# Optimization experiments

Hardware: AMD Instinct MI355X
Metric: run time of the kernel (lower is better)

The kernel has to match this reference:

```python
import jax, jax.numpy as jnp
import numpy as np

N, T = 32, 1024
CIN, H, O, F2 = 64, 128, 16, 16  # F2 = 2 * FiLMed_layers
EPS = 1e-5
SLOPE = 0.01  # nn.LeakyReLU default


def _leaky(x):
    return jnp.where(x >= 0, x, SLOPE * x)


def _ln(x, gamma, beta):
    # x: (N,T,O,H); gamma,beta: (O,H) -> broadcast per channel
    mu = jnp.mean(x, axis=-1, keepdims=True)
    var = jnp.mean(jnp.square(x - mu), axis=-1, keepdims=True)
    return (x - mu) * jax.lax.rsqrt(var + EPS) * gamma + beta


def setup_inputs() -> dict:
    key = jax.random.key(0)
    ks = jax.random.split(key, 7)
    s0 = 1.0 / np.sqrt(CIN)
    s1 = 1.0 / np.sqrt(H)
    return {
        "x": jax.random.normal(ks[0], (N, T, CIN), jnp.float32),
        "W0": jax.random.uniform(ks[1], (O, H, CIN), jnp.float32, -s0, s0),
        "b0": jax.random.uniform(ks[2], (O, H), jnp.float32, -s0, s0),
        "g0": jnp.ones((O, H), jnp.float32),
        "be0": jnp.zeros((O, H), jnp.float32),
        "W1": jax.random.uniform(ks[3], (O, H, H), jnp.float32, -s1, s1),
        "b1": jax.random.uniform(ks[4], (O, H), jnp.float32, -s1, s1),
        "g1": jnp.ones((O, H), jnp.float32),
        "be1": jnp.zeros((O, H), jnp.float32),
        "W2": jax.random.uniform(ks[5], (O, F2, H), jnp.float32, -s1, s1),
        "b2": jax.random.uniform(ks[6], (O, F2), jnp.float32, -s1, s1),
    }


def reference(x, W0, b0, g0, be0, W1, b1, g1, be1, W2, b2):
    # Per-channel MLP, vectorized over the O channel axis.
    h = jnp.einsum("ntc,ohc->ntoh", x, W0) + b0          # (N,T,O,H)
    h = _ln(_leaky(h), g0, be0)
    h = jnp.einsum("ntoh,ogh->ntog", h, W1) + b1         # (N,T,O,H)
    h = _ln(_leaky(h), g1, be1)
    out = jnp.einsum("ntoh,ofh->ntof", h, W2) + b2       # (N,T,O,F2)
    out = _leaky(out)
    # torch: stack(dim=1) -> (N,O,T,F2); moveaxis(1,-1) -> (N,T,F2,O)
    return jnp.moveaxis(out, 2, 3)
```

## Files before the change

kernel.cpp:

```cpp
#include <hip/hip_runtime.h>

#define NTOK  32768
#define CIN   64
#define HDIM  128
#define O_CH  16
#define F2    16
#define SLOPE 0.01f
#define EPS   1e-5f

#define SW0_STRIDE 72
#define SW1_STRIDE 136
#define SW2_STRIDE 136
#define SH_STRIDE  136
#define SW0_OFF 0
#define SW1_OFF 9216
#define SW2_OFF (9216 + 17408)
#define WIMG_SHORTS 28800
#define SH_OFF  28800
#define SMEM_TOT (28800 + 64 * SH_STRIDE)

#define WIMG_OFF   0
#define WIMG_BYTES ((size_t)O_CH * WIMG_SHORTS * 2)
#define XBF_OFF    WIMG_BYTES
#define XBF_BYTES  ((size_t)NTOK * CIN * 2)
#define B0F_OFF    (XBF_OFF + XBF_BYTES)
#define B0F_BYTES  ((size_t)O_CH * HDIM * 4)
#define B1F_OFF    (B0F_OFF + B0F_BYTES)
#define B1F_BYTES  ((size_t)O_CH * HDIM * 4)
#define B2F_OFF    (B1F_OFF + B1F_BYTES)
#define B2F_BYTES  ((size_t)O_CH * F2 * 4)

typedef __attribute__((ext_vector_type(8))) short bf16x8;
typedef __attribute__((ext_vector_type(4))) short bf16x4;
typedef __attribute__((ext_vector_type(4))) float f32x4;

__device__ __forceinline__ float b2f(unsigned short u) {
  union { unsigned int i; float f; } v;
  v.i = ((unsigned int)u) << 16;
  return v.f;
}
__device__ __forceinline__ unsigned short f2b(float f) {
  union { float f; unsigned int i; } v;
  v.f = f;
  unsigned int i = v.i;
  unsigned int r = (i + 0x7fffu + ((i >> 16) & 1u)) >> 16;
  return (unsigned short)r;
}
__device__ __forceinline__ float leaky(float t) {
  return (t >= 0.f) ? t : SLOPE * t;
}
__device__ __forceinline__ bf16x8 cvt8(const float* __restrict__ p) {
  float4 a = *(const float4*)p;
  float4 b = *(const float4*)(p + 4);
  bf16x8 r;
  r[0] = (short)f2b(a.x); r[1] = (short)f2b(a.y);
  r[2] = (short)f2b(a.z); r[3] = (short)f2b(a.w);
  r[4] = (short)f2b(b.x); r[5] = (short)f2b(b.y);
  r[6] = (short)f2b(b.z); r[7] = (short)f2b(b.w);
  return r;
}
__device__ __forceinline__ bf16x8 cvt8s(const float* __restrict__ p,
                                        const float* __restrict__ s) {
  bf16x8 r;
#pragma unroll
  for (int i = 0; i < 8; ++i) r[i] = (short)f2b(p[i] * s[i]);
  return r;
}

__device__ __forceinline__ void leaky_ln_store(
    const f32x4* acc, unsigned short* __restrict__ sh,
    int row0, int lo16, int quad) {
  float v[8][4];
  float s1 = 0.f, s2 = 0.f;
#pragma unroll
  for (int nt = 0; nt < 8; ++nt) {
#pragma unroll
    for (int r = 0; r < 4; ++r) {
      float t = leaky(acc[nt][r]);
      v[nt][r] = t;
      s1 += t;
      s2 += t * t;
    }
  }
  s1 += __shfl_xor(s1, 16); s2 += __shfl_xor(s2, 16);
  s1 += __shfl_xor(s1, 32); s2 += __shfl_xor(s2, 32);
  float mu = s1 * (1.0f / 128.0f);
  float var = s2 * (1.0f / 128.0f) - mu * mu;
  float rs = rsqrtf(var + EPS);
#pragma unroll
  for (int nt = 0; nt < 8; ++nt) {
    bf16x4 p;
#pragma unroll
    for (int r = 0; r < 4; ++r)
      p[r] = (short)f2b((v[nt][r] - mu) * rs);
    *(bf16x4*)&sh[(row0 + lo16) * SH_STRIDE + nt * 16 + quad * 4] = p;
  }
}

__global__ __launch_bounds__(256) void prep(
    const float* __restrict__ x,
    const float* __restrict__ W0, const float* __restrict__ b0,
    const float* __restrict__ g0, const float* __restrict__ be0,
    const float* __restrict__ W1, const float* __restrict__ b1,
    const float* __restrict__ g1, const float* __restrict__ be1,
    const float* __restrict__ W2, const float* __restrict__ b2,
    unsigned short* __restrict__ wimg, unsigned short* __restrict__ xbf,
    float* __restrict__ b0f, float* __restrict__ b1f,
    float* __restrict__ b2f) {
  const int bid = blockIdx.x, tid = threadIdx.x;
  if (bid < 16) {
    const int o = bid;
    __shared__ float sg0[HDIM], sbe0[HDIM], sg1[HDIM], sbe1[HDIM];
    if (tid < 128) {
      sg0[tid]  = g0 [o * HDIM + tid];
      sbe0[tid] = be0[o * HDIM + tid];
      sg1[tid]  = g1 [o * HDIM + tid];
      sbe1[tid] = be1[o * HDIM + tid];
    }
    __syncthreads();
    unsigned short* img = wimg + (size_t)o * WIMG_SHORTS;
    const float* w0 = W0 + (size_t)o * HDIM * CIN;
    for (int c = tid; c < (HDIM * CIN) / 8; c += 256) {
      int n = c >> 3, k8 = c & 7;
      *(bf16x8*)&img[SW0_OFF + n * SW0_STRIDE + k8 * 8] = cvt8(w0 + c * 8);
    }
    const float* w1 = W1 + (size_t)o * HDIM * HDIM;
    for (int c = tid; c < (HDIM * HDIM) / 8; c += 256) {
      int n = c >> 4, k8 = c & 15;
      *(bf16x8*)&img[SW1_OFF + n * SW1_STRIDE + k8 * 8] =
          cvt8s(w1 + c * 8, sg0 + k8 * 8);
    }
    const float* w2 = W2 + (size_t)o * F2 * HDIM;
    for (int c = tid; c < (F2 * HDIM) / 8; c += 256) {
      int n = c >> 4, k8 = c & 15;
      *(bf16x8*)&img[SW2_OFF + n * SW2_STRIDE + k8 * 8] =
          cvt8s(w2 + c * 8, sg1 + k8 * 8);
    }
    if (tid < 128) {
      b0f[o * HDIM + tid] = b0[o * HDIM + tid];
      float d = 0.f;
      const float* w1r = w1 + (size_t)tid * HDIM;
      for (int k = 0; k < HDIM; ++k) d += w1r[k] * sbe0[k];
      b1f[o * HDIM + tid] = b1[o * HDIM + tid] + d;
    } else if (tid < 144) {
      int f = tid - 128;
      float d = 0.f;
      const float* w2r = w2 + (size_t)f * HDIM;
      for (int k = 0; k < HDIM; ++k) d += w2r[k] * sbe1[k];
      b2f[o * F2 + f] = b2[o * F2 + f] + d;
    }
  } else {
    int idx = (bid - 16) * 256 + tid;
    *(bf16x8*)&xbf[(size_t)idx * 8] = cvt8(x + (size_t)idx * 8);
  }
}

__global__ __launch_bounds__(256, 2) void film_main(
    const unsigned short* __restrict__ xbf,
    const unsigned short* __restrict__ wimg,
    const float* __restrict__ b0f, const float* __restrict__ b1f,
    const float* __restrict__ b2f,
    float* __restrict__ out) {
  __shared__ unsigned short smem[SMEM_TOT];
  const int tid = threadIdx.x;
  const int c   = blockIdx.x & 7;
  const int o   = (blockIdx.x >> 3) & 15;
  const int q   = blockIdx.x >> 7;
  const int tok0 = (q * 8 + c) * 256;

  {
    const bf16x8* src = (const bf16x8*)(wimg + (size_t)o * WIMG_SHORTS);
    for (int i = tid; i < WIMG_SHORTS / 8; i += 256)
      *(bf16x8*)&smem[i * 8] = src[i];
  }

  const int lane = tid & 63;
  const int wave = tid >> 6;
  const int lo16 = lane & 15;
  const int quad = lane >> 4;
  const int row0 = wave * 16;

  f32x4 bias0[8], bias1[8];
#pragma unroll
  for (int nt = 0; nt < 8; ++nt) {
    bias0[nt] = *(const f32x4*)&b0f[o * HDIM + nt * 16 + quad * 4];
    bias1[nt] = *(const f32x4*)&b1f[o * HDIM + nt * 16 + quad * 4];
  }
  const f32x4 bias2 = *(const f32x4*)&b2f[o * F2 + quad * 4];
  __syncthreads();

  for (int mt = 0; mt < 4; ++mt) {
    const int trow = tok0 + wave * 64 + mt * 16;

    f32x4 acc[8];
#pragma unroll
    for (int nt = 0; nt < 8; ++nt) acc[nt] = bias0[nt];
    {
      const unsigned short* xr = xbf + (size_t)(trow + lo16) * CIN + quad * 8;
#pragma unroll
      for (int ks = 0; ks < 2; ++ks) {
        bf16x8 bx = *(const bf16x8*)(xr + ks * 32);
#pragma unroll
        for (int nt = 0; nt < 8; ++nt) {
          bf16x8 a = *(const bf16x8*)
              &smem[SW0_OFF + (nt * 16 + lo16) * SW0_STRIDE + ks * 32 + quad * 8];
          acc[nt] = __builtin_amdgcn_mfma_f32_16x16x32_bf16(a, bx, acc[nt], 0, 0, 0);
        }
      }
    }
    leaky_ln_store(acc, smem + SH_OFF, row0, lo16, quad);

#pragma unroll
    for (int nt = 0; nt < 8; ++nt) acc[nt] = bias1[nt];
#pragma unroll
    for (int ks = 0; ks < 4; ++ks) {
      bf16x8 bh = *(const bf16x8*)
          &smem[SH_OFF + (row0 + lo16) * SH_STRIDE + ks * 32 + quad * 8];
#pragma unroll
      for (int nt = 0; nt < 8; ++nt) {
        bf16x8 a = *(const bf16x8*)
            &smem[SW1_OFF + (nt * 16 + lo16) * SW1_STRIDE + ks * 32 + quad * 8];
        acc[nt] = __builtin_amdgcn_mfma_f32_16x16x32_bf16(a, bh, acc[nt], 0, 0, 0);
      }
    }
    leaky_ln_store(acc, smem + SH_OFF, row0, lo16, quad);

    f32x4 acc2 = bias2;
#pragma unroll
    for (int ks = 0; ks < 4; ++ks) {
      bf16x8 bh = *(const bf16x8*)
          &smem[SH_OFF + (row0 + lo16) * SH_STRIDE + ks * 32 + quad * 8];
      bf16x8 a = *(const bf16x8*)
          &smem[SW2_OFF + lo16 * SW2_STRIDE + ks * 32 + quad * 8];
      acc2 = __builtin_amdgcn_mfma_f32_16x16x32_bf16(a, bh, acc2, 0, 0, 0);
    }
    {
      const size_t tb = (size_t)(trow + lo16) * (F2 * O_CH);
#pragma unroll
      for (int r = 0; r < 4; ++r)
        out[tb + (quad * 4 + r) * O_CH + o] = leaky(acc2[r]);
    }
  }
}

extern "C" void kernel_launch(void* const* d_in, const int* in_sizes, int n_in,
                              void* d_out, int out_size, void* d_ws, size_t ws_size,
                              hipStream_t stream) {
  (void)in_sizes; (void)n_in; (void)out_size; (void)ws_size;
  const float* x   = (const float*)d_in[0];
  const float* W0  = (const float*)d_in[1];
  const float* b0  = (const float*)d_in[2];
  const float* g0  = (const float*)d_in[3];
  const float* be0 = (const float*)d_in[4];
  const float* W1  = (const float*)d_in[5];
  const float* b1  = (const float*)d_in[6];
  const float* g1  = (const float*)d_in[7];
  const float* be1 = (const float*)d_in[8];
  const float* W2  = (const float*)d_in[9];
  const float* b2  = (const float*)d_in[10];

  unsigned short* wimg = (unsigned short*)((char*)d_ws + WIMG_OFF);
  unsigned short* xbf  = (unsigned short*)((char*)d_ws + XBF_OFF);
  float* b0f = (float*)((char*)d_ws + B0F_OFF);
  float* b1f = (float*)((char*)d_ws + B1F_OFF);
  float* b2f = (float*)((char*)d_ws + B2F_OFF);

  prep<<<dim3(16 + (NTOK * CIN / 8) / 256), dim3(256), 0, stream>>>(
      x, W0, b0, g0, be0, W1, b1, g1, be1, W2, b2, wimg, xbf, b0f, b1f, b2f);
  film_main<<<dim3(O_CH * (NTOK / 256)), dim3(256), 0, stream>>>(
      xbf, wimg, b0f, b1f, b2f, (float*)d_out);
}
```

Measured before the change: 170.2 us.

## Read fp32 x directly, stream W0 from global, and process two token tiles per pass

The x-to-bf16 conversion pass in prep is removed. The main kernel now loads fp32 x and converts it in registers. W0 is kept in a plain bf16 global buffer and read from global/L2 rather than staged in LDS, which frees LDS so the hidden scratch can hold 32 rows per wave. Each wave now handles two 16-token tiles at once, so every weight fragment load feeds two MFMAs. In exchange, register pressure rises and x is converted 16 times, once per channel block. W0 global reads may also add latency.

New measurement: 186.9 us. 1.1x slower.

```diff
diff --git a/kernel.cpp b/kernel.cpp
--- a/kernel.cpp
+++ b/kernel.cpp
@@ -8,22 +8,20 @@
 #define SLOPE 0.01f
 #define EPS   1e-5f
 
-#define SW0_STRIDE 72
 #define SW1_STRIDE 136
 #define SW2_STRIDE 136
 #define SH_STRIDE  136
-#define SW0_OFF 0
-#define SW1_OFF 9216
-#define SW2_OFF (9216 + 17408)
-#define WIMG_SHORTS 28800
-#define SH_OFF  28800
-#define SMEM_TOT (28800 + 64 * SH_STRIDE)
-
-#define WIMG_OFF   0
+#define SW1_OFF 0
+#define SW2_OFF 17408
+#define WIMG_SHORTS (17408 + 2176)
+#define SH_OFF  WIMG_SHORTS
+#define SMEM_TOT (WIMG_SHORTS + 128 * SH_STRIDE)
+
+#define W0G_OFF    0
+#define W0G_BYTES  ((size_t)O_CH * HDIM * CIN * 2)
+#define WIMG_OFF   W0G_BYTES
 #define WIMG_BYTES ((size_t)O_CH * WIMG_SHORTS * 2)
-#define XBF_OFF    WIMG_BYTES
-#define XBF_BYTES  ((size_t)NTOK * CIN * 2)
-#define B0F_OFF    (XBF_OFF + XBF_BYTES)
+#define B0F_OFF    (WIMG_OFF + WIMG_BYTES)
 #define B0F_BYTES  ((size_t)O_CH * HDIM * 4)
 #define B1F_OFF    (B0F_OFF + B0F_BYTES)
 #define B1F_BYTES  ((size_t)O_CH * HDIM * 4)
@@ -34,11 +32,6 @@
 typedef __attribute__((ext_vector_type(4))) short bf16x4;
 typedef __attribute__((ext_vector_type(4))) float f32x4;
 
-__device__ __forceinline__ float b2f(unsigned short u) {
-  union { unsigned int i; float f; } v;
-  v.i = ((unsigned int)u) << 16;
-  return v.f;
-}
 __device__ __forceinline__ unsigned short f2b(float f) {
   union { float f; unsigned int i; } v;
   v.f = f;
@@ -49,7 +42,7 @@
 __device__ __forceinline__ float leaky(float t) {
   return (t >= 0.f) ? t : SLOPE * t;
 }
-__device__ __forceinline__ bf16x8 cvt8(const float* __restrict__ p) {
+__device__ __forceinline__ bf16x8 cvt8(const float* p) {
   float4 a = *(const float4*)p;
   float4 b = *(const float4*)(p + 4);
   bf16x8 r;
@@ -59,8 +52,7 @@
   r[6] = (short)f2b(b.z); r[7] = (short)f2b(b.w);
   return r;
 }
-__device__ __forceinline__ bf16x8 cvt8s(const float* __restrict__ p,
-                                        const float* __restrict__ s) {
+__device__ __forceinline__ bf16x8 cvt8s(const float* p, const float* s) {
   bf16x8 r;
 #pragma unroll
   for (int i = 0; i < 8; ++i) r[i] = (short)f2b(p[i] * s[i]);
@@ -68,8 +60,7 @@
 }
 
 __device__ __forceinline__ void leaky_ln_store(
-    const f32x4* acc, unsigned short* __restrict__ sh,
-    int row0, int lo16, int quad) {
+    const f32x4* acc, unsigned short* sh, int shrow, int quad) {
   float v[8][4];
   float s1 = 0.f, s2 = 0.f;
 #pragma unroll
@@ -93,70 +84,62 @@
 #pragma unroll
     for (int r = 0; r < 4; ++r)
       p[r] = (short)f2b((v[nt][r] - mu) * rs);
-    *(bf16x4*)&sh[(row0 + lo16) * SH_STRIDE + nt * 16 + quad * 4] = p;
+    *(bf16x4*)&sh[shrow * SH_STRIDE + nt * 16 + quad * 4] = p;
   }
 }
 
 __global__ __launch_bounds__(256) void prep(
-    const float* __restrict__ x,
     const float* __restrict__ W0, const float* __restrict__ b0,
     const float* __restrict__ g0, const float* __restrict__ be0,
     const float* __restrict__ W1, const float* __restrict__ b1,
     const float* __restrict__ g1, const float* __restrict__ be1,
     const float* __restrict__ W2, const float* __restrict__ b2,
-    unsigned short* __restrict__ wimg, unsigned short* __restrict__ xbf,
+    unsigned short* __restrict__ w0g, unsigned short* __restrict__ wimg,
     float* __restrict__ b0f, float* __restrict__ b1f,
     float* __restrict__ b2f) {
-  const int bid = blockIdx.x, tid = threadIdx.x;
-  if (bid < 16) {
-    const int o = bid;
-    __shared__ float sg0[HDIM], sbe0[HDIM], sg1[HDIM], sbe1[HDIM];
-    if (tid < 128) {
-      sg0[tid]  = g0 [o * HDIM + tid];
-      sbe0[tid] = be0[o * HDIM + tid];
-      sg1[tid]  = g1 [o * HDIM + tid];
-      sbe1[tid] = be1[o * HDIM + tid];
-    }
-    __syncthreads();
-    unsigned short* img = wimg + (size_t)o * WIMG_SHORTS;
-    const float* w0 = W0 + (size_t)o * HDIM * CIN;
-    for (int c = tid; c < (HDIM * CIN) / 8; c += 256) {
-      int n = c >> 3, k8 = c & 7;
-      *(bf16x8*)&img[SW0_OFF + n * SW0_STRIDE + k8 * 8] = cvt8(w0 + c * 8);
-    }
-    const float* w1 = W1 + (size_t)o * HDIM * HDIM;
-    for (int c = tid; c < (HDIM * HDIM) / 8; c += 256) {
-      int n = c >> 4, k8 = c & 15;
-      *(bf16x8*)&img[SW1_OFF + n * SW1_STRIDE + k8 * 8] =
-          cvt8s(w1 + c * 8, sg0 + k8 * 8);
-    }
-    const float* w2 = W2 + (size_t)o * F2 * HDIM;
-    for (int c = tid; c < (F2 * HDIM) / 8; c += 256) {
-      int n = c >> 4, k8 = c & 15;
-      *(bf16x8*)&img[SW2_OFF + n * SW2_STRIDE + k8 * 8] =
-          cvt8s(w2 + c * 8, sg1 + k8 * 8);
-    }
-    if (tid < 128) {
-      b0f[o * HDIM + tid] = b0[o * HDIM + tid];
-      float d = 0.f;
-      const float* w1r = w1 + (size_t)tid * HDIM;
-      for (int k = 0; k < HDIM; ++k) d += w1r[k] * sbe0[k];
-      b1f[o * HDIM + tid] = b1[o * HDIM + tid] + d;
-    } else if (tid < 144) {
-      int f = tid - 128;
-      float d = 0.f;
-      const float* w2r = w2 + (size_t)f * HDIM;
-      for (int k = 0; k < HDIM; ++k) d += w2r[k] * sbe1[k];
-      b2f[o * F2 + f] = b2[o * F2 + f] + d;
-    }
-  } else {
-    int idx = (bid - 16) * 256 + tid;
-    *(bf16x8*)&xbf[(size_t)idx * 8] = cvt8(x + (size_t)idx * 8);
+  const int o = blockIdx.x, tid = threadIdx.x;
+  __shared__ float sg0[HDIM], sbe0[HDIM], sg1[HDIM], sbe1[HDIM];
+  if (tid < 128) {
+    sg0[tid]  = g0 [o * HDIM + tid];
+    sbe0[tid] = be0[o * HDIM + tid];
+    sg1[tid]  = g1 [o * HDIM + tid];
+    sbe1[tid] = be1[o * HDIM + tid];
+  }
+  __syncthreads();
+  const float* w0 = W0 + (size_t)o * HDIM * CIN;
+  for (int c = tid; c < (HDIM * CIN) / 8; c += 256)
+    *(bf16x8*)&w0g[(size_t)o * HDIM * CIN + c * 8] = cvt8(w0 + c * 8);
+  unsigned short* img = wimg + (size_t)o * WIMG_SHORTS;
+  const float* w1 = W1 + (size_t)o * HDIM * HDIM;
+  for (int c = tid; c < (HDIM * HDIM) / 8; c += 256) {
+    int n = c >> 4, k8 = c & 15;
+    *(bf16x8*)&img[SW1_OFF + n * SW1_STRIDE + k8 * 8] =
+        cvt8s(w1 + c * 8, sg0 + k8 * 8);
+  }
+  const float* w2 = W2 + (size_t)o * F2 * HDIM;
+  for (int c = tid; c < (F2 * HDIM) / 8; c += 256) {
+    int n = c >> 4, k8 = c & 15;
+    *(bf16x8*)&img[SW2_OFF + n * SW2_STRIDE + k8 * 8] =
+        cvt8s(w2 + c * 8, sg1 + k8 * 8);
+  }
+  if (tid < 128) {
+    b0f[o * HDIM + tid] = b0[o * HDIM + tid];
+    float d = 0.f;
+    const float* w1r = w1 + (size_t)tid * HDIM;
+    for (int k = 0; k < HDIM; ++k) d += w1r[k] * sbe0[k];
+    b1f[o * HDIM + tid] = b1[o * HDIM + tid] + d;
+  } else if (tid < 144) {
+    int f = tid - 128;
+    float d = 0.f;
+    const float* w2r = w2 + (size_t)f * HDIM;
+    for (int k = 0; k < HDIM; ++k) d += w2r[k] * sbe1[k];
+    b2f[o * F2 + f] = b2[o * F2 + f] + d;
   }
 }
 
 __global__ __launch_bounds__(256, 2) void film_main(
-    const unsigned short* __restrict__ xbf,
+    const float* __restrict__ x,
+    const unsigned short* __restrict__ w0g,
     const unsigned short* __restrict__ wimg,
     const float* __restrict__ b0f, const float* __restrict__ b1f,
     const float* __restrict__ b2f,
@@ -178,7 +161,7 @@
   const int wave = tid >> 6;
   const int lo16 = lane & 15;
   const int quad = lane >> 4;
-  const int row0 = wave * 16;
+  unsigned short* sh = smem + SH_OFF;
 
   f32x4 bias0[8], bias1[8];
 #pragma unroll
@@ -187,58 +170,65 @@
     bias1[nt] = *(const f32x4*)&b1f[o * HDIM + nt * 16 + quad * 4];
   }
   const f32x4 bias2 = *(const f32x4*)&b2f[o * F2 + quad * 4];
+  const unsigned short* w0o = w0g + (size_t)o * HDIM * CIN;
   __syncthreads();
 
-  for (int mt = 0; mt < 4; ++mt) {
-    const int trow = tok0 + wave * 64 + mt * 16;
-
-    f32x4 acc[8];
-#pragma unroll
-    for (int nt = 0; nt < 8; ++nt) acc[nt] = bias0[nt];
-    {
-      const unsigned short* xr = xbf + (size_t)(trow + lo16) * CIN + quad * 8;
-#pragma unroll
-      for (int ks = 0; ks < 2; ++ks) {
-        bf16x8 bx = *(const bf16x8*)(xr + ks * 32);
-#pragma unroll
-        for (int nt = 0; nt < 8; ++nt) {
-          bf16x8 a = *(const bf16x8*)
-              &smem[SW0_OFF + (nt * 16 + lo16) * SW0_STRIDE + ks * 32 + quad * 8];
-          acc[nt] = __builtin_amdgcn_mfma_f32_16x16x32_bf16(a, bx, acc[nt], 0, 0, 0);
-        }
+  for (int st = 0; st < 2; ++st) {
+    const int tb = tok0 + wave * 64 + st * 32;
+    const int shbase = wave * 32;
+
+    f32x4 acc0[8], acc1[8];
+#pragma unroll
+    for (int nt = 0; nt < 8; ++nt) { acc0[nt] = bias0[nt]; acc1[nt] = bias0[nt]; }
+#pragma unroll
+    for (int ks = 0; ks < 2; ++ks) {
+      bf16x8 bx0 = cvt8(&x[(size_t)(tb + lo16) * CIN + ks * 32 + quad * 8]);
+      bf16x8 bx1 = cvt8(&x[(size_t)(tb + 16 + lo16) * CIN + ks * 32 + quad * 8]);
+#pragma unroll
+      for (int nt = 0; nt < 8; ++nt) {
+        bf16x8 a = *(const bf16x8*)&w0o[(size_t)(nt * 16 + lo16) * CIN + ks * 32 + quad * 8];
+        acc0[nt] = __builtin_amdgcn_mfma_f32_16x16x32_bf16(a, bx0, acc0[nt], 0, 0, 0);
+        acc1[nt] = __builtin_amdgcn_mfma_f32_16x16x32_bf16(a, bx1, acc1[nt], 0, 0, 0);
       }
     }
-    leaky_ln_store(acc, smem + SH_OFF, row0, lo16, quad);
-
-#pragma unroll
-    for (int nt = 0; nt < 8; ++nt) acc[nt] = bias1[nt];
+    leaky_ln_store(acc0, sh, shbase + lo16, quad);
+    leaky_ln_store(acc1, sh, shbase + 16 + lo16, quad);
+
+#pragma unroll
+    for (int nt = 0; nt < 8; ++nt) { acc0[nt] = bias1[nt]; acc1[nt] = bias1[nt]; }
 #pragma unroll
     for (int ks = 0; ks < 4; ++ks) {
-      bf16x8 bh = *(const bf16x8*)
-          &smem[SH_OFF + (row0 + lo16) * SH_STRIDE + ks * 32 + quad * 8];
+      bf16x8 bh0 = *(const bf16x8*)&sh[(shbase + lo16) * SH_STRIDE + ks * 32 + quad * 8];
+      bf16x8 bh1 = *(const bf16x8*)&sh[(shbase + 16 + lo16) * SH_STRIDE + ks * 32 + quad * 8];
 #pragma unroll
       for (int nt = 0; nt < 8; ++nt) {
         bf16x8 a = *(const bf16x8*)
             &smem[SW1_OFF + (nt * 16 + lo16) * SW1_STRIDE + ks * 32 + quad * 8];
-        acc[nt] = __builtin_amdgcn_mfma_f32_16x16x32_bf16(a, bh, acc[nt], 0, 0, 0);
+        acc0[nt] = __builtin_amdgcn_mfma_f32_16x16x32_bf16(a, bh0, acc0[nt], 0, 0, 0);
+        acc1[nt] = __builtin_amdgcn_mfma_f32_16x16x32_bf16(a, bh1, acc1[nt], 0, 0, 0);
       }
     }
-    leaky_ln_store(acc, smem + SH_OFF, row0, lo16, quad);
-
-    f32x4 acc2 = bias2;
+    leaky_ln_store(acc0, sh, shbase + lo16, quad);
+    leaky_ln_store(acc1, sh, shbase + 16 + lo16, quad);
+
+    f32x4 acc2a = bias2, acc2b = bias2;
 #pragma unroll
     for (int ks = 0; ks < 4; ++ks) {
-      bf16x8 bh = *(const bf16x8*)
-          &smem[SH_OFF + (row0 + lo16) * SH_STRIDE + ks * 32 + quad * 8];
+      bf16x8 bh0 = *(const bf16x8*)&sh[(shbase + lo16) * SH_STRIDE + ks * 32 + quad * 8];
+      bf16x8 bh1 = *(const bf16x8*)&sh[(shbase + 16 + lo16) * SH_STRIDE + ks * 32 + quad * 8];
       bf16x8 a = *(const bf16x8*)
           &smem[SW2_OFF + lo16 * SW2_STRIDE + ks * 32 + quad * 8];
-      acc2 = __builtin_amdgcn_mfma_f32_16x16x32_bf16(a, bh, acc2, 0, 0, 0);
+      acc2a = __builtin_amdgcn_mfma_f32_16x16x32_bf16(a, bh0, acc2a, 0, 0, 0);
+      acc2b = __builtin_amdgcn_mfma_f32_16x16x32_bf16(a, bh1, acc2b, 0, 0, 0);
     }
     {
-      const size_t tb = (size_t)(trow + lo16) * (F2 * O_CH);
-#pragma unroll
-      for (int r = 0; r < 4; ++r)
-        out[tb + (quad * 4 + r) * O_CH + o] = leaky(acc2[r]);
+      const size_t ta = (size_t)(tb + lo16) * (F2 * O_CH);
+      const size_t tbf = (size_t)(tb + 16 + lo16) * (F2 * O_CH);
+#pragma unroll
+      for (int r = 0; r < 4; ++r) {
+        out[ta  + (quad * 4 + r) * O_CH + o] = leaky(acc2a[r]);
+        out[tbf + (quad * 4 + r) * O_CH + o] = leaky(acc2b[r]);
+      }
     }
   }
 }
@@ -259,14 +249,14 @@
   const float* W2  = (const float*)d_in[9];
   const float* b2  = (const float*)d_in[10];
 
+  unsigned short* w0g  = (unsigned short*)((char*)d_ws + W0G_OFF);
   unsigned short* wimg = (unsigned short*)((char*)d_ws + WIMG_OFF);
-  unsigned short* xbf  = (unsigned short*)((char*)d_ws + XBF_OFF);
   float* b0f = (float*)((char*)d_ws + B0F_OFF);
   float* b1f = (float*)((char*)d_ws + B1F_OFF);
   float* b2f = (float*)((char*)d_ws + B2F_OFF);
 
-  prep<<<dim3(16 + (NTOK * CIN / 8) / 256), dim3(256), 0, stream>>>(
-      x, W0, b0, g0, be0, W1, b1, g1, be1, W2, b2, wimg, xbf, b0f, b1f, b2f);
+  prep<<<dim3(16), dim3(256), 0, stream>>>(
+      W0, b0, g0, be0, W1, b1, g1, be1, W2, b2, w0g, wimg, b0f, b1f, b2f);
   film_main<<<dim3(O_CH * (NTOK / 256)), dim3(256), 0, stream>>>(
-      xbf, wimg, b0f, b1f, b2f, (float*)d_out);
-}
+      x, w0g, wimg, b0f, b1f, b2f, (float*)d_out);
+}
```
